# Kernel tuning notes

Measured on AMD Instinct MI355X. Metric: run time of the kernel, lower is better.

## Reference

```python
import jax, jax.numpy as jnp
import numpy as np

B, N, D, H = 32, 64, 256, 256
WORD_NUM, REL_NUM, POS_NUM, CAT_NUM = 50000, 50, 48, 5


def setup_inputs() -> dict:
    key = jax.random.key(0)
    ks = jax.random.split(key, 20)
    rng = np.random.default_rng(0)
    # valid dependency trees: head[i] < i, head[0] = -1 (root)
    heads_np = np.zeros((B, N), dtype=np.int32)
    for b in range(B):
        heads_np[b, 0] = -1
        for i in range(1, N):
            heads_np[b, i] = rng.integers(0, i)
    p = lambda k, shape: (0.02 * jax.random.normal(k, shape)).astype(jnp.float32)
    z = lambda shape: jnp.zeros(shape, jnp.float32)
    return {
        "xs": jax.random.randint(ks[0], (B, N), 0, WORD_NUM),
        "heads": jnp.asarray(heads_np),
        "rels": jax.random.randint(ks[1], (B, N), 0, REL_NUM),
        "labels": jax.random.randint(ks[2], (B, N), 0, WORD_NUM),
        "poss": jax.random.randint(ks[3], (B, N), 0, POS_NUM),
        "xlengths": jnp.full((B,), N, dtype=jnp.int32),
        "target_start": jnp.zeros((B,), jnp.int32),
        "target_end": jnp.full((B,), N - 1, jnp.int32),
        "x_mask": jnp.ones((B, N), jnp.float32),
        # parameters
        "emb_W": p(ks[4], (WORD_NUM, D)),
        "rel_W": p(ks[5], (REL_NUM, D)),
        "gru_Wi_f": p(ks[6], (2 * D, 3 * H)), "gru_Wh_f": p(ks[7], (H, 3 * H)),
        "gru_bi_f": z((3 * H,)), "gru_bh_f": z((3 * H,)),
        "gru_Wi_b": p(ks[8], (2 * D, 3 * H)), "gru_Wh_b": p(ks[9], (H, 3 * H)),
        "gru_bi_b": z((3 * H,)), "gru_bh_b": z((3 * H,)),
        "Wt": p(ks[10], (2 * H, D)), "bt": z((D,)),
        "dt_Wx": p(ks[11], (2 * D, 3 * H)), "dt_Uh": p(ks[12], (H, 3 * H)), "dt_b": z((3 * H,)),
        "td_Wx": p(ks[13], (2 * D, 3 * H)), "td_Uh": p(ks[14], (H, 3 * H)), "td_b": z((3 * H,)),
        "fc_W": p(ks[15], (2 * H, 100)), "fc_b": z((100,)),
        "fc2_W": p(ks[16], (100, CAT_NUM)), "fc2_b": z((CAT_NUM,)),
    }


def _gru_cell(xpt, hprev, Uh, bh):
    gh = hprev @ Uh + bh
    xr, xz, xn = jnp.split(xpt, 3, axis=-1)
    hr, hz, hn = jnp.split(gh, 3, axis=-1)
    r = jax.nn.sigmoid(xr + hr)
    zg = jax.nn.sigmoid(xz + hz)
    n = jnp.tanh(xn + r * hn)
    return (1.0 - zg) * n + zg * hprev


def _gru_dir(x, Wi, Wh, bi, bh):
    # x: [B,N,2D] -> hidden sequence [B,N,H]
    xp = x @ Wi + bi  # precompute input projections
    def step(h, xpt):
        hnew = _gru_cell(xpt, h, Wh, bh)
        return hnew, hnew
    h0 = jnp.zeros((x.shape[0], Wh.shape[0]), x.dtype)
    _, hs = jax.lax.scan(step, h0, jnp.swapaxes(xp, 0, 1))
    return jnp.swapaxes(hs, 0, 1)


def _dt_tree(inputs, heads, Wx, Uh, b):
    # bottom-up (child-sum) tree GRU; heads[b,i] < i so reversed order is topological
    Bn, Nn, _ = inputs.shape
    Hh = Uh.shape[0]
    xp = inputs @ Wx + b
    bar = jnp.arange(Bn)
    def step(carry, idx):
        C, Hout = carry  # C: accumulated child hidden sums [B,N,H]
        h = _gru_cell(xp[:, idx], C[:, idx], Uh, jnp.zeros((3 * Hh,), inputs.dtype))
        Hout = Hout.at[:, idx].set(h)
        par = heads[:, idx]
        valid = par >= 0
        C = C.at[bar, jnp.where(valid, par, 0)].add(jnp.where(valid[:, None], h, 0.0))
        return (C, Hout), None
    H0 = jnp.zeros((Bn, Nn, Hh), inputs.dtype)
    (_, Hout), _ = jax.lax.scan(step, (H0, H0), jnp.arange(Nn - 1, -1, -1))
    return Hout


def _td_tree(inputs, heads, Wx, Uh, b):
    # top-down tree GRU: parent hidden flows to children; index order 0..N-1 is topological
    Bn, Nn, _ = inputs.shape
    Hh = Uh.shape[0]
    xp = inputs @ Wx + b
    bar = jnp.arange(Bn)
    def step(Hout, idx):
        par = heads[:, idx]
        valid = par >= 0
        hp = jnp.where(valid[:, None], Hout[bar, jnp.where(valid, par, 0)], 0.0)
        h = _gru_cell(xp[:, idx], hp, Uh, jnp.zeros((3 * Hh,), inputs.dtype))
        Hout = Hout.at[:, idx].set(h)
        return Hout, None
    H0 = jnp.zeros((Bn, Nn, Hh), inputs.dtype)
    Hout, _ = jax.lax.scan(step, H0, jnp.arange(Nn))
    return Hout


def reference(xs, heads, rels, labels, poss, xlengths, target_start, target_end, x_mask,
              emb_W, rel_W,
              gru_Wi_f, gru_Wh_f, gru_bi_f, gru_bh_f,
              gru_Wi_b, gru_Wh_b, gru_bi_b, gru_bh_b,
              Wt, bt, dt_Wx, dt_Uh, dt_b, td_Wx, td_Uh, td_b,
              fc_W, fc_b, fc2_W, fc2_b):
    word_emb = emb_W[xs]
    label_emb = emb_W[labels]  # original uses self.embedding for labels too
    emb = jnp.concatenate([word_emb, label_emb], axis=-1)  # [B,N,2D]
    fwd = _gru_dir(emb, gru_Wi_f, gru_Wh_f, gru_bi_f, gru_bh_f)
    bwd = jnp.flip(_gru_dir(jnp.flip(emb, 1), gru_Wi_b, gru_Wh_b, gru_bi_b, gru_bh_b), 1)
    grus = jnp.concatenate([fwd, bwd], axis=-1) @ Wt + bt  # transform -> [B,N,D]
    rel_emb = rel_W[rels]
    outputs = jnp.concatenate([grus, rel_emb], axis=-1)  # [B,N,2D]
    dt_out = _dt_tree(outputs, heads, dt_Wx, dt_Uh, dt_b)
    td_out = _td_tree(outputs, heads, td_Wx, td_Uh, td_b)
    ctx = jnp.concatenate([dt_out, td_out], axis=-1)  # [B,N,2H]
    ctx = jnp.max(ctx, axis=1)  # max_pool1d over length -> [B,2H]
    ctx = ctx @ fc_W + fc_b
    ctx = ctx @ fc2_W + fc2_b
    return ctx
```

## Files before the change

### kernel.cpp

```cpp
#include <hip/hip_runtime.h>


typedef _Float16 half2v __attribute__((ext_vector_type(2)));
typedef _Float16 half8 __attribute__((ext_vector_type(8)));
typedef unsigned int u32x32 __attribute__((ext_vector_type(32)));
typedef float f32x4v __attribute__((ext_vector_type(4)));

__device__ __forceinline__ float fdot2f(unsigned a, unsigned b, float c) {
#if __has_builtin(__builtin_amdgcn_fdot2)
  return __builtin_amdgcn_fdot2(__builtin_bit_cast(half2v, a),
                                __builtin_bit_cast(half2v, b), c, false);
#else
  half2v av = __builtin_bit_cast(half2v, a), bv = __builtin_bit_cast(half2v, b);
  return c + (float)av.x * (float)bv.x + (float)av.y * (float)bv.y;
#endif
}

__device__ __forceinline__ unsigned packh2(float x, float y) {
  half2v p;
  p.x = (_Float16)x;
  p.y = (_Float16)y;
  return __builtin_bit_cast(unsigned, p);
}
__device__ __forceinline__ unsigned short f2u(float x) {
  return __builtin_bit_cast(unsigned short, (_Float16)x);
}
__device__ __forceinline__ float sigm(float x) { return 1.f / (1.f + __expf(-x)); }
__device__ __forceinline__ float tanh_fast(float x) {
  float cx = fminf(fmaxf(x, -15.f), 15.f);
  float e = __expf(2.f * cx);
  return (e - 1.f) / (e + 1.f);
}

__global__ __launch_bounds__(256) void pack_w(const float* __restrict__ W0,
                                              const float* __restrict__ W1,
                                              const float* __restrict__ W2,
                                              const float* __restrict__ W3, unsigned* P0,
                                              unsigned* P1, unsigned* P2, unsigned* P3) {
  const float* W;
  unsigned* P;
  switch (blockIdx.y) {
    case 0: W = W0; P = P0; break;
    case 1: W = W1; P = P1; break;
    case 2: W = W2; P = P2; break;
    default: W = W3; P = P3; break;
  }
  const int tid = blockIdx.x * 256 + threadIdx.x;
  const int i = tid & 3;
  const int u4 = tid >> 2;
  const int jg = u4 & 127;
  const int d4q = u4 >> 7;
  const int d4 = d4q % 48;
  const int q2 = d4q / 48;
  const int col2 = d4 / 24;
  const int rr = d4 % 24;
  const int g = rr >> 3;
  const int p4 = rr & 7;
  const int kp = p4 * 4 + i;
  const int k = q2 * 64 + kp * 2;
  const int col = g * 256 + col2 * 128 + jg;
  P[tid] = packh2(W[(size_t)k * 768 + col], W[(size_t)(k + 1) * 768 + col]);
}

__global__ __launch_bounds__(256) void tsplit(const float* __restrict__ W,
                                              unsigned short* __restrict__ WThi,
                                              unsigned short* __restrict__ WTlo, int K,
                                              int N) {
  __shared__ float T[32][33];
  const int ky = blockIdx.y * 32, nx = blockIdx.x * 32;
  const int r = threadIdx.x >> 3, c4 = (threadIdx.x & 7) * 4;
  float4 v = *(const float4*)(W + (size_t)(ky + r) * N + nx + c4);
  T[r][c4 + 0] = v.x;
  T[r][c4 + 1] = v.y;
  T[r][c4 + 2] = v.z;
  T[r][c4 + 3] = v.w;
  __syncthreads();
  float f[4] = {T[c4 + 0][r], T[c4 + 1][r], T[c4 + 2][r], T[c4 + 3][r]};
  ushort4 oh, ol;
  {
    _Float16 h0 = (_Float16)f[0], h1 = (_Float16)f[1], h2 = (_Float16)f[2],
             h3 = (_Float16)f[3];
    oh.x = __builtin_bit_cast(unsigned short, h0);
    oh.y = __builtin_bit_cast(unsigned short, h1);
    oh.z = __builtin_bit_cast(unsigned short, h2);
    oh.w = __builtin_bit_cast(unsigned short, h3);
    ol.x = f2u(f[0] - (float)h0);
    ol.y = f2u(f[1] - (float)h1);
    ol.z = f2u(f[2] - (float)h2);
    ol.w = f2u(f[3] - (float)h3);
  }
  *(ushort4*)(WThi + (size_t)(nx + r) * K + ky + c4) = oh;
  *(ushort4*)(WTlo + (size_t)(nx + r) * K + ky + c4) = ol;
}

__global__ void gather_emb_hl(const int* __restrict__ xs, const int* __restrict__ labels,
                              const float* __restrict__ embW,
                              unsigned short* __restrict__ eHi,
                              unsigned short* __restrict__ eLo) {
  const int row = blockIdx.x, t = threadIdx.x;
  const float4* W4 = (const float4*)embW;
  const int src = (t < 64) ? xs[row] : labels[row];
  float4 v = W4[(size_t)src * 64 + (t & 63)];
  float f[4] = {v.x, v.y, v.z, v.w};
  ushort4 oh, ol;
  _Float16 h0 = (_Float16)f[0], h1 = (_Float16)f[1], h2 = (_Float16)f[2],
           h3 = (_Float16)f[3];
  oh.x = __builtin_bit_cast(unsigned short, h0);
  oh.y = __builtin_bit_cast(unsigned short, h1);
  oh.z = __builtin_bit_cast(unsigned short, h2);
  oh.w = __builtin_bit_cast(unsigned short, h3);
  ol.x = f2u(f[0] - (float)h0);
  ol.y = f2u(f[1] - (float)h1);
  ol.z = f2u(f[2] - (float)h2);
  ol.w = f2u(f[3] - (float)h3);
  const size_t idx = (size_t)row * 512 + (t >> 6) * 256 + (t & 63) * 4;
  *(ushort4*)(eHi + idx) = oh;
  *(ushort4*)(eLo + idx) = ol;
}

__global__ void gather_rel_hl(const int* __restrict__ rels,
                              const float* __restrict__ relW,
                              unsigned short* __restrict__ oHi,
                              unsigned short* __restrict__ oLo) {
  const int row = blockIdx.x, t = threadIdx.x;
  const float4* W4 = (const float4*)relW;
  float4 v = W4[(size_t)rels[row] * 64 + t];
  float f[4] = {v.x, v.y, v.z, v.w};
  ushort4 oh, ol;
  _Float16 h0 = (_Float16)f[0], h1 = (_Float16)f[1], h2 = (_Float16)f[2],
           h3 = (_Float16)f[3];
  oh.x = __builtin_bit_cast(unsigned short, h0);
  oh.y = __builtin_bit_cast(unsigned short, h1);
  oh.z = __builtin_bit_cast(unsigned short, h2);
  oh.w = __builtin_bit_cast(unsigned short, h3);
  ol.x = f2u(f[0] - (float)h0);
  ol.y = f2u(f[1] - (float)h1);
  ol.z = f2u(f[2] - (float)h2);
  ol.w = f2u(f[3] - (float)h3);
  const size_t idx = (size_t)row * 512 + 256 + t * 4;
  *(ushort4*)(oHi + idx) = oh;
  *(ushort4*)(oLo + idx) = ol;
}

__global__ __launch_bounds__(256) void mm16p(
    const unsigned short* __restrict__ Ahi, const unsigned short* __restrict__ Alo,
    const unsigned short* __restrict__ Bhi, const unsigned short* __restrict__ Blo,
    const float* __restrict__ bias, float* __restrict__ Cf,
    unsigned short* __restrict__ CHi, unsigned short* __restrict__ CLo, int ldc,
    int mode) {
  __shared__ __align__(16) _Float16 As_h[64][40], As_l[64][40];
  __shared__ __align__(16) _Float16 Bs_h[64][40], Bs_l[64][40];
  const int t = threadIdx.x, l = t & 63, w = t >> 6;
  const int bm = blockIdx.y * 64, bn = blockIdx.x * 64;
  const int sr = t >> 2, sc = (t & 3) * 8;
  f32x4v ac0 = {0.f, 0.f, 0.f, 0.f}, ac1 = ac0, ac2 = ac0, ac3 = ac0;
  const int fr = w * 16 + (l & 15), fc = (l >> 4) * 8, lo16 = l & 15;
  for (int kt = 0; kt < 512; kt += 32) {
    *(uint4*)(&As_h[sr][sc]) = *(const uint4*)(Ahi + (size_t)(bm + sr) * 512 + kt + sc);
    *(uint4*)(&As_l[sr][sc]) = *(const uint4*)(Alo + (size_t)(bm + sr) * 512 + kt + sc);
    *(uint4*)(&Bs_h[sr][sc]) = *(const uint4*)(Bhi + (size_t)(bn + sr) * 512 + kt + sc);
    *(uint4*)(&Bs_l[sr][sc]) = *(const uint4*)(Blo + (size_t)(bn + sr) * 512 + kt + sc);
    __syncthreads();
    half8 avh = __builtin_bit_cast(half8, *(const uint4*)(&As_h[fr][fc]));
    half8 avl = __builtin_bit_cast(half8, *(const uint4*)(&As_l[fr][fc]));
#define BH(NT) __builtin_bit_cast(half8, *(const uint4*)(&Bs_h[(NT)*16 + lo16][fc]))
#define BL(NT) __builtin_bit_cast(half8, *(const uint4*)(&Bs_l[(NT)*16 + lo16][fc]))
    half8 b0h = BH(0), b1h = BH(1), b2h = BH(2), b3h = BH(3);
    half8 b0l = BL(0), b1l = BL(1), b2l = BL(2), b3l = BL(3);
#undef BH
#undef BL
    ac0 = __builtin_amdgcn_mfma_f32_16x16x32_f16(avh, b0h, ac0, 0, 0, 0);
    ac1 = __builtin_amdgcn_mfma_f32_16x16x32_f16(avh, b1h, ac1, 0, 0, 0);
    ac2 = __builtin_amdgcn_mfma_f32_16x16x32_f16(avh, b2h, ac2, 0, 0, 0);
    ac3 = __builtin_amdgcn_mfma_f32_16x16x32_f16(avh, b3h, ac3, 0, 0, 0);
    ac0 = __builtin_amdgcn_mfma_f32_16x16x32_f16(avh, b0l, ac0, 0, 0, 0);
    ac1 = __builtin_amdgcn_mfma_f32_16x16x32_f16(avh, b1l, ac1, 0, 0, 0);
    ac2 = __builtin_amdgcn_mfma_f32_16x16x32_f16(avh, b2l, ac2, 0, 0, 0);
    ac3 = __builtin_amdgcn_mfma_f32_16x16x32_f16(avh, b3l, ac3, 0, 0, 0);
    ac0 = __builtin_amdgcn_mfma_f32_16x16x32_f16(avl, b0h, ac0, 0, 0, 0);
    ac1 = __builtin_amdgcn_mfma_f32_16x16x32_f16(avl, b1h, ac1, 0, 0, 0);
    ac2 = __builtin_amdgcn_mfma_f32_16x16x32_f16(avl, b2h, ac2, 0, 0, 0);
    ac3 = __builtin_amdgcn_mfma_f32_16x16x32_f16(avl, b3h, ac3, 0, 0, 0);
    __syncthreads();
  }
  const int hi4 = l >> 4;
#define EPI(AC, NT)                                                            \
  {                                                                            \
    _Pragma("unroll") for (int i = 0; i < 4; ++i) {                            \
      const int row = bm + w * 16 + hi4 * 4 + i;                               \
      const int col = bn + (NT)*16 + lo16;                                     \
      float v = (AC)[i] + bias[col];                                           \
      if (mode == 0) {                                                         \
        Cf[(size_t)row * ldc + col] = v;                                       \
      } else {                                                                 \
        _Float16 h = (_Float16)v;                                              \
        CHi[(size_t)row * ldc + col] = __builtin_bit_cast(unsigned short, h);  \
        CLo[(size_t)row * ldc + col] = f2u(v - (float)h);                      \
      }                                                                        \
    }                                                                          \
  }
  EPI(ac0, 0) EPI(ac1, 1) EPI(ac2, 2) EPI(ac3, 3)
#undef EPI
}

__global__ __launch_bounds__(256) void mm16s_wt(const float* __restrict__ A,
                                                const float* __restrict__ W,
                                                const float* __restrict__ bias,
                                                unsigned short* __restrict__ CHi,
                                                unsigned short* __restrict__ CLo, int N,
                                                int ldc) {
  __shared__ __align__(16) _Float16 Ahi[64][40], Alo[64][40];
  __shared__ __align__(16) _Float16 Bhi[64][40], Blo[64][40];
  const int t = threadIdx.x, l = t & 63, w = t >> 6;
  const int bm = blockIdx.y * 64, bn = blockIdx.x * 64;
  const int ar = t >> 2, ac8 = (t & 3) * 8;
  const int bk = t >> 3, bn8 = (t & 7) * 8;
  f32x4v ac0 = {0.f, 0.f, 0.f, 0.f}, ac1 = ac0, ac2 = ac0, ac3 = ac0;
  const int fr = w * 16 + (l & 15), fc = (l >> 4) * 8, lo16 = l & 15;
  for (int kt = 0; kt < 512; kt += 32) {
    {
      const float* ap = A + (size_t)(bm + ar) * 512 + kt + ac8;
      float4 v0 = *(const float4*)ap;
      float4 v1 = *(const float4*)(ap + 4);
      float av[8] = {v0.x, v0.y, v0.z, v0.w, v1.x, v1.y, v1.z, v1.w};
#pragma unroll
      for (int i = 0; i < 8; ++i) {
        _Float16 h = (_Float16)av[i];
        Ahi[ar][ac8 + i] = h;
        Alo[ar][ac8 + i] = (_Float16)(av[i] - (float)h);
      }
    }
    {
      const float* wp = W + (size_t)(kt + bk) * N + bn + bn8;
      float4 v0 = *(const float4*)wp;
      float4 v1 = *(const float4*)(wp + 4);
      float wv[8] = {v0.x, v0.y, v0.z, v0.w, v1.x, v1.y, v1.z, v1.w};
#pragma unroll
      for (int i = 0; i < 8; ++i) {
        _Float16 h = (_Float16)wv[i];
        Bhi[bn8 + i][bk] = h;
        Blo[bn8 + i][bk] = (_Float16)(wv[i] - (float)h);
      }
    }
    __syncthreads();
    half8 avh = __builtin_bit_cast(half8, *(const uint4*)(&Ahi[fr][fc]));
    half8 avl = __builtin_bit_cast(half8, *(const uint4*)(&Alo[fr][fc]));
#define BH(NT) __builtin_bit_cast(half8, *(const uint4*)(&Bhi[(NT)*16 + lo16][fc]))
#define BL(NT) __builtin_bit_cast(half8, *(const uint4*)(&Blo[(NT)*16 + lo16][fc]))
    half8 b0h = BH(0), b1h = BH(1), b2h = BH(2), b3h = BH(3);
    half8 b0l = BL(0), b1l = BL(1), b2l = BL(2), b3l = BL(3);
#undef BH
#undef BL
    ac0 = __builtin_amdgcn_mfma_f32_16x16x32_f16(avh, b0h, ac0, 0, 0, 0);
    ac1 = __builtin_amdgcn_mfma_f32_16x16x32_f16(avh, b1h, ac1, 0, 0, 0);
    ac2 = __builtin_amdgcn_mfma_f32_16x16x32_f16(avh, b2h, ac2, 0, 0, 0);
    ac3 = __builtin_amdgcn_mfma_f32_16x16x32_f16(avh, b3h, ac3, 0, 0, 0);
    ac0 = __builtin_amdgcn_mfma_f32_16x16x32_f16(avh, b0l, ac0, 0, 0, 0);
    ac1 = __builtin_amdgcn_mfma_f32_16x16x32_f16(avh, b1l, ac1, 0, 0, 0);
    ac2 = __builtin_amdgcn_mfma_f32_16x16x32_f16(avh, b2l, ac2, 0, 0, 0);
    ac3 = __builtin_amdgcn_mfma_f32_16x16x32_f16(avh, b3l, ac3, 0, 0, 0);
    ac0 = __builtin_amdgcn_mfma_f32_16x16x32_f16(avl, b0h, ac0, 0, 0, 0);
    ac1 = __builtin_amdgcn_mfma_f32_16x16x32_f16(avl, b1h, ac1, 0, 0, 0);
    ac2 = __builtin_amdgcn_mfma_f32_16x16x32_f16(avl, b2h, ac2, 0, 0, 0);
    ac3 = __builtin_amdgcn_mfma_f32_16x16x32_f16(avl, b3h, ac3, 0, 0, 0);
    __syncthreads();
  }
  const int hi4 = l >> 4;
#define EPI(AC, NT)                                                            \
  {                                                                            \
    _Pragma("unroll") for (int i = 0; i < 4; ++i) {                            \
      const int row = bm + w * 16 + hi4 * 4 + i;                               \
      const int col = bn + (NT)*16 + lo16;                                     \
      float v = (AC)[i] + bias[col];                                           \
      _Float16 h = (_Float16)v;                                                \
      CHi[(size_t)row * ldc + col] = __builtin_bit_cast(unsigned short, h);    \
      CLo[(size_t)row * ldc + col] = f2u(v - (float)h);                        \
    }                                                                          \
  }
  EPI(ac0, 0) EPI(ac1, 1) EPI(ac2, 2) EPI(ac3, 3)
#undef EPI
}

template <int NP>
__device__ __forceinline__ void stage_w(const uint4* __restrict__ P4, int q2, int jg,
                                        int t, uint2 (*Wl)[512], u32x32& w0, u32x32& w1,
                                        u32x32& w2) {
#pragma unroll
  for (int p4 = 0; p4 < 8; ++p4) {
    uint4 v0 = P4[(q2 * 48 + p4) * 128 + jg];
    w0[4 * p4 + 0] = v0.x; w0[4 * p4 + 1] = v0.y;
    w0[4 * p4 + 2] = v0.z; w0[4 * p4 + 3] = v0.w;
    uint4 v1 = P4[(q2 * 48 + 8 + p4) * 128 + jg];
    w1[4 * p4 + 0] = v1.x; w1[4 * p4 + 1] = v1.y;
    w1[4 * p4 + 2] = v1.z; w1[4 * p4 + 3] = v1.w;
    uint4 v2 = P4[(q2 * 48 + 16 + p4) * 128 + jg];
    w2[4 * p4 + 0] = v2.x; w2[4 * p4 + 1] = v2.y;
    w2[4 * p4 + 2] = v2.z; w2[4 * p4 + 3] = v2.w;
  }
#pragma unroll
  for (int g = 0; g < 3; ++g)
#pragma unroll
    for (int p4 = 0; p4 < NP; ++p4) {
      uint4 v = P4[(q2 * 48 + 24 + g * 8 + p4) * 128 + jg];
      Wl[(g * NP + p4) * 2 + 0][t] = make_uint2(v.x, v.y);
      Wl[(g * NP + p4) * 2 + 1][t] = make_uint2(v.z, v.w);
    }
}

template <int NP>
__device__ __forceinline__ void dot_step(const u32x32& w0, const u32x32& w1,
                                         const u32x32& w2, const uint2 (*Wl)[512], int t,
                                         const uint4* __restrict__ P4, int sb,
                                         const uint4* hv4, float& a0, float& a1,
                                         float& a2, float& a3, float& a4, float& a5) {
#pragma unroll
  for (int c = 0; c < 8; ++c) {
    uint4 hu = hv4[c];
    a0 = fdot2f(w0[4 * c + 0], hu.x, a0); a0 = fdot2f(w0[4 * c + 1], hu.y, a0);
    a0 = fdot2f(w0[4 * c + 2], hu.z, a0); a0 = fdot2f(w0[4 * c + 3], hu.w, a0);
    a1 = fdot2f(w1[4 * c + 0], hu.x, a1); a1 = fdot2f(w1[4 * c + 1], hu.y, a1);
    a1 = fdot2f(w1[4 * c + 2], hu.z, a1); a1 = fdot2f(w1[4 * c + 3], hu.w, a1);
    a2 = fdot2f(w2[4 * c + 0], hu.x, a2); a2 = fdot2f(w2[4 * c + 1], hu.y, a2);
    a2 = fdot2f(w2[4 * c + 2], hu.z, a2); a2 = fdot2f(w2[4 * c + 3], hu.w, a2);
    if (c < NP) {
      uint2 u0 = Wl[(0 * NP + c) * 2 + 0][t], u1 = Wl[(0 * NP + c) * 2 + 1][t];
      a3 = fdot2f(u0.x, hu.x, a3); a3 = fdot2f(u0.y, hu.y, a3);
      a3 = fdot2f(u1.x, hu.z, a3); a3 = fdot2f(u1.y, hu.w, a3);
      uint2 v0 = Wl[(1 * NP + c) * 2 + 0][t], v1 = Wl[(1 * NP + c) * 2 + 1][t];
      a4 = fdot2f(v0.x, hu.x, a4); a4 = fdot2f(v0.y, hu.y, a4);
      a4 = fdot2f(v1.x, hu.z, a4); a4 = fdot2f(v1.y, hu.w, a4);
      uint2 x0 = Wl[(2 * NP + c) * 2 + 0][t], x1 = Wl[(2 * NP + c) * 2 + 1][t];
      a5 = fdot2f(x0.x, hu.x, a5); a5 = fdot2f(x0.y, hu.y, a5);
      a5 = fdot2f(x1.x, hu.z, a5); a5 = fdot2f(x1.y, hu.w, a5);
    } else {
      uint4 s0 = P4[sb + (0 * 8 + c) * 128];
      a3 = fdot2f(s0.x, hu.x, a3); a3 = fdot2f(s0.y, hu.y, a3);
      a3 = fdot2f(s0.z, hu.z, a3); a3 = fdot2f(s0.w, hu.w, a3);
      uint4 s1 = P4[sb + (1 * 8 + c) * 128];
      a4 = fdot2f(s1.x, hu.x, a4); a4 = fdot2f(s1.y, hu.y, a4);
      a4 = fdot2f(s1.z, hu.z, a4); a4 = fdot2f(s1.w, hu.w, a4);
      uint4 s2 = P4[sb + (2 * 8 + c) * 128];
      a5 = fdot2f(s2.x, hu.x, a5); a5 = fdot2f(s2.y, hu.y, a5);
      a5 = fdot2f(s2.z, hu.z, a5); a5 = fdot2f(s2.w, hu.w, a5);
    }
  }
}

__global__ __launch_bounds__(512) void gru_scan_h(
    const unsigned* __restrict__ Pf, const unsigned* __restrict__ Pb,
    const float* __restrict__ bh_f, const float* __restrict__ bh_b,
    const float* __restrict__ xp_f, const float* __restrict__ xp_b,
    float* __restrict__ grus) {
  const int b = blockIdx.x & 31, dir = blockIdx.x >> 5;
  const uint4* __restrict__ P4 = (const uint4*)(dir ? Pb : Pf);
  const float* __restrict__ bh = dir ? bh_b : bh_f;
  const float* __restrict__ xp = dir ? xp_b : xp_f;

  __shared__ uint2 Wl[36][512];
  __shared__ float part[4][3][256];
  __shared__ __align__(16) unsigned h2[128];

  const int t = threadIdx.x, jg = t & 127, q2 = t >> 7;
  const int sb = (q2 * 48 + 24) * 128 + jg;

  u32x32 w0, w1, w2;
  stage_w<6>(P4, q2, jg, t, Wl, w0, w1, w2);

  float br0 = 0.f, br1 = 0.f, bz0 = 0.f, bz1 = 0.f, bn0 = 0.f, bn1 = 0.f;
  float hp0 = 0.f, hp1 = 0.f;
  if (t < 128) {
    br0 = bh[2 * t];       br1 = bh[2 * t + 1];
    bz0 = bh[256 + 2 * t]; bz1 = bh[256 + 2 * t + 1];
    bn0 = bh[512 + 2 * t]; bn1 = bh[512 + 2 * t + 1];
    h2[t] = 0u;
  }
  __syncthreads();

  for (int s = 0; s < 64; ++s) {
    const int nn = dir ? (63 - s) : s;
    float2 pxr, pxz, pxn;
    if (t < 128) {
      const float* xrow = xp + (size_t)(b * 64 + nn) * 768;
      pxr = *(const float2*)(xrow + 2 * t);
      pxz = *(const float2*)(xrow + 256 + 2 * t);
      pxn = *(const float2*)(xrow + 512 + 2 * t);
    }
    float a0 = 0.f, a1 = 0.f, a2 = 0.f, a3 = 0.f, a4 = 0.f, a5 = 0.f;
    dot_step<6>(w0, w1, w2, Wl, t, P4, sb, (const uint4*)(h2 + q2 * 32), a0, a1, a2, a3,
                a4, a5);
    part[q2][0][jg] = a0;
    part[q2][0][128 + jg] = a3;
    part[q2][1][jg] = a1;
    part[q2][1][128 + jg] = a4;
    part[q2][2][jg] = a2;
    part[q2][2][128 + jg] = a5;
    __syncthreads();
    if (t < 128) {
      float s0r = 0, s1r = 0, s0z = 0, s1z = 0, s0n = 0, s1n = 0;
#pragma unroll
      for (int q = 0; q < 4; ++q) {
        float2 pr = *(const float2*)(&part[q][0][2 * t]); s0r += pr.x; s1r += pr.y;
        float2 pz = *(const float2*)(&part[q][1][2 * t]); s0z += pz.x; s1z += pz.y;
        float2 pn = *(const float2*)(&part[q][2][2 * t]); s0n += pn.x; s1n += pn.y;
      }
      float r0 = sigm(pxr.x + s0r + br0), r1 = sigm(pxr.y + s1r + br1);
      float z0 = sigm(pxz.x + s0z + bz0), z1 = sigm(pxz.y + s1z + bz1);
      float n0 = tanh_fast(pxn.x + r0 * (s0n + bn0));
      float n1 = tanh_fast(pxn.y + r1 * (s1n + bn1));
      float h0 = (1.f - z0) * n0 + z0 * hp0;
      float h1 = (1.f - z1) * n1 + z1 * hp1;
      hp0 = h0;
      hp1 = h1;
      h2[t] = packh2(h0, h1);
      float2 o;
      o.x = h0;
      o.y = h1;
      *(float2*)(grus + (size_t)(b * 64 + nn) * 512 + dir * 256 + 2 * t) = o;
    }
    __syncthreads();
  }
}

__global__ __launch_bounds__(512) void tree_scan_h(
    const unsigned* __restrict__ Pdt, const unsigned* __restrict__ Ptd,
    const float* __restrict__ xp_dt, const float* __restrict__ xp_td,
    const int* __restrict__ heads, float* __restrict__ ctx) {
  const int b = blockIdx.x & 31, istd = blockIdx.x >> 5;
  const uint4* __restrict__ P4 = (const uint4*)(istd ? Ptd : Pdt);
  const float* __restrict__ xp = istd ? xp_td : xp_dt;

  __shared__ float S[65][256];
  __shared__ __align__(16) unsigned S2[65][128];
  __shared__ uint2 Wl[12][512];
  __shared__ float part[4][3][256];
  __shared__ int hd[64];

  const int t = threadIdx.x, jg = t & 127, q2 = t >> 7;
  const int sb = (q2 * 48 + 24) * 128 + jg;

  u32x32 w0, w1, w2;
  stage_w<2>(P4, q2, jg, t, Wl, w0, w1, w2);

  for (int i = t; i < 65 * 256; i += 512) (&S[0][0])[i] = 0.f;
  for (int i = t; i < 65 * 128; i += 512) (&S2[0][0])[i] = 0u;
  if (t < 64) hd[t] = heads[b * 64 + t];
  __syncthreads();

  float mx0 = -1e30f, mx1 = -1e30f;

  for (int s = 0; s < 64; ++s) {
    const int idx = istd ? s : (63 - s);
    const int par = hd[idx];
    const int srow = istd ? (par >= 0 ? par : 64) : idx;

    float2 pxr, pxz, pxn;
    if (t < 128) {
      const float* xrow = xp + (size_t)(b * 64 + idx) * 768;
      pxr = *(const float2*)(xrow + 2 * t);
      pxz = *(const float2*)(xrow + 256 + 2 * t);
      pxn = *(const float2*)(xrow + 512 + 2 * t);
    }
    float a0 = 0.f, a1 = 0.f, a2 = 0.f, a3 = 0.f, a4 = 0.f, a5 = 0.f;
    dot_step<2>(w0, w1, w2, Wl, t, P4, sb, (const uint4*)(&S2[srow][q2 * 32]), a0, a1,
                a2, a3, a4, a5);
    part[q2][0][jg] = a0;
    part[q2][0][128 + jg] = a3;
    part[q2][1][jg] = a1;
    part[q2][1][128 + jg] = a4;
    part[q2][2][jg] = a2;
    part[q2][2][128 + jg] = a5;
    __syncthreads();
    if (t < 128) {
      float s0r = 0, s1r = 0, s0z = 0, s1z = 0, s0n = 0, s1n = 0;
#pragma unroll
      for (int q = 0; q < 4; ++q) {
        float2 pr = *(const float2*)(&part[q][0][2 * t]); s0r += pr.x; s1r += pr.y;
        float2 pz = *(const float2*)(&part[q][1][2 * t]); s0z += pz.x; s1z += pz.y;
        float2 pn = *(const float2*)(&part[q][2][2 * t]); s0n += pn.x; s1n += pn.y;
      }
      float r0 = sigm(pxr.x + s0r), r1 = sigm(pxr.y + s1r);
      float z0 = sigm(pxz.x + s0z), z1 = sigm(pxz.y + s1z);
      float n0 = tanh_fast(pxn.x + r0 * s0n), n1 = tanh_fast(pxn.y + r1 * s1n);
      float hp0 = S[srow][2 * t], hp1 = S[srow][2 * t + 1];
      float h0 = (1.f - z0) * n0 + z0 * hp0;
      float h1 = (1.f - z1) * n1 + z1 * hp1;
      mx0 = fmaxf(mx0, h0);
      mx1 = fmaxf(mx1, h1);
      if (istd) {
        S[idx][2 * t] = h0;
        S[idx][2 * t + 1] = h1;
        S2[idx][t] = packh2(h0, h1);
      } else if (par >= 0) {
        float c0 = S[par][2 * t] + h0;
        float c1 = S[par][2 * t + 1] + h1;
        S[par][2 * t] = c0;
        S[par][2 * t + 1] = c1;
        S2[par][t] = packh2(c0, c1);
      }
    }
    __syncthreads();
  }

  if (t < 128) {
    float2 o;
    o.x = mx0;
    o.y = mx1;
    *(float2*)(ctx + (size_t)b * 512 + istd * 256 + 2 * t) = o;
  }
}

__global__ __launch_bounds__(128) void final_k(const float* __restrict__ ctx_g,
                                               const float* __restrict__ fcW,
                                               const float* __restrict__ fcb,
                                               const float* __restrict__ fc2W,
                                               const float* __restrict__ fc2b,
                                               float* __restrict__ out) {
  const int b = blockIdx.x, t = threadIdx.x;
  __shared__ float ctx[512];
  __shared__ float f1[100];
  for (int i = t; i < 512; i += 128) ctx[i] = ctx_g[(size_t)b * 512 + i];
  __syncthreads();
  if (t < 100) {
    float a = fcb[t];
    for (int k = 0; k < 512; ++k) a = fmaf(ctx[k], fcW[k * 100 + t], a);
    f1[t] = a;
  }
  __syncthreads();
  if (t < 5) {
    float a = fc2b[t];
    for (int k = 0; k < 100; ++k) a = fmaf(f1[k], fc2W[k * 5 + t], a);
    out[b * 5 + t] = a;
  }
}

extern "C" void kernel_launch(void* const* d_in, const int* in_sizes, int n_in, void* d_out,
                              int out_size, void* d_ws, size_t ws_size, hipStream_t stream) {
  const int* xs = (const int*)d_in[0];
  const int* heads = (const int*)d_in[1];
  const int* rels = (const int*)d_in[2];
  const int* labels = (const int*)d_in[3];
  const float* emb_W = (const float*)d_in[9];
  const float* rel_W = (const float*)d_in[10];
  const float* Wi_f = (const float*)d_in[11];
  const float* Wh_f = (const float*)d_in[12];
  const float* bi_f = (const float*)d_in[13];
  const float* bh_f = (const float*)d_in[14];
  const float* Wi_b = (const float*)d_in[15];
  const float* Wh_b = (const float*)d_in[16];
  const float* bi_b = (const float*)d_in[17];
  const float* bh_b = (const float*)d_in[18];
  const float* Wt = (const float*)d_in[19];
  const float* bt = (const float*)d_in[20];
  const float* dt_Wx = (const float*)d_in[21];
  const float* dt_Uh = (const float*)d_in[22];
  const float* dt_b = (const float*)d_in[23];
  const float* td_Wx = (const float*)d_in[24];
  const float* td_Uh = (const float*)d_in[25];
  const float* td_b = (const float*)d_in[26];
  const float* fc_W = (const float*)d_in[27];
  const float* fc_b = (const float*)d_in[28];
  const float* fc2_W = (const float*)d_in[29];
  const float* fc2_b = (const float*)d_in[30];

  float* ws = (float*)d_ws;
  float* xp_f = ws;
  float* xp_b = ws + 1572864;
  float* grus = ws + 3145728;
  float* ctx = ws + 4194304;
  unsigned* P0 = (unsigned*)(ws + 4210688);
  unsigned* P1 = P0 + 98304;
  unsigned* P2 = P1 + 98304;
  unsigned* P3 = P2 + 98304;
  unsigned short* embHi = (unsigned short*)(ws + 4603904);
  unsigned short* embLo = (unsigned short*)(ws + 5128192);
  unsigned short* WTh_a = (unsigned short*)(ws + 5652480);
  unsigned short* WTl_a = (unsigned short*)(ws + 5849088);
  unsigned short* WTh_b = (unsigned short*)(ws + 6045696);
  unsigned short* WTl_b = (unsigned short*)(ws + 6242304);
  unsigned short* outHi = embHi;
  unsigned short* outLo = embLo;

  pack_w<<<dim3(384, 4), 256, 0, stream>>>(Wh_f, Wh_b, dt_Uh, td_Uh, P0, P1, P2, P3);
  tsplit<<<dim3(24, 16), 256, 0, stream>>>(Wi_f, WTh_a, WTl_a, 512, 768);
  tsplit<<<dim3(24, 16), 256, 0, stream>>>(Wi_b, WTh_b, WTl_b, 512, 768);
  gather_emb_hl<<<2048, 128, 0, stream>>>(xs, labels, emb_W, embHi, embLo);
  mm16p<<<dim3(12, 32), 256, 0, stream>>>(embHi, embLo, WTh_a, WTl_a, bi_f, xp_f,
                                          nullptr, nullptr, 768, 0);
  mm16p<<<dim3(12, 32), 256, 0, stream>>>(embHi, embLo, WTh_b, WTl_b, bi_b, xp_b,
                                          nullptr, nullptr, 768, 0);
  gru_scan_h<<<64, 512, 0, stream>>>(P0, P1, bh_f, bh_b, xp_f, xp_b, grus);
  tsplit<<<dim3(24, 16), 256, 0, stream>>>(dt_Wx, WTh_a, WTl_a, 512, 768);
  tsplit<<<dim3(24, 16), 256, 0, stream>>>(td_Wx, WTh_b, WTl_b, 512, 768);
  mm16s_wt<<<dim3(4, 32), 256, 0, stream>>>(grus, Wt, bt, outHi, outLo, 256, 512);
  gather_rel_hl<<<2048, 64, 0, stream>>>(rels, rel_W, outHi, outLo);
  mm16p<<<dim3(12, 32), 256, 0, stream>>>(outHi, outLo, WTh_a, WTl_a, dt_b, xp_f,
                                          nullptr, nullptr, 768, 0);
  mm16p<<<dim3(12, 32), 256, 0, stream>>>(outHi, outLo, WTh_b, WTl_b, td_b, xp_b,
                                          nullptr, nullptr, 768, 0);
  tree_scan_h<<<64, 512, 0, stream>>>(P2, P3, xp_f, xp_b, heads, ctx);
  final_k<<<32, 128, 0, stream>>>(ctx, fc_W, fc_b, fc2_W, fc2_b, (float*)d_out);
}
```

Baseline: 328.0 us.

## Move tree-scan fp32 state to global memory to stage more weights in LDS

The tree scan kernel's fp32 hidden-state array S moves from shared memory to a per-block global workspace. The freed LDS holds twice as many recurrent weight slices (stage_w/dot_step<4>), which cuts per-step global weight reads. The prior-state loads are issued before the dot product so their latency overlaps the matvec. Separately, the paired tsplit launches are merged into one launch using blockIdx.z. The risk is that global-memory round trips for state on the serial dependency chain add latency, and the Sg workspace reuses the embHi region that is no longer needed.

Result: no change. 325.8 us (-0.7%).

```diff
diff --git a/kernel.cpp b/kernel.cpp
--- a/kernel.cpp
+++ b/kernel.cpp
@@ -62,10 +62,16 @@
   P[tid] = packh2(W[(size_t)k * 768 + col], W[(size_t)(k + 1) * 768 + col]);
 }
 
-__global__ __launch_bounds__(256) void tsplit(const float* __restrict__ W,
-                                              unsigned short* __restrict__ WThi,
-                                              unsigned short* __restrict__ WTlo, int K,
-                                              int N) {
+__global__ __launch_bounds__(256) void tsplit2(const float* __restrict__ W0,
+                                               const float* __restrict__ W1,
+                                               unsigned short* __restrict__ H0,
+                                               unsigned short* __restrict__ L0,
+                                               unsigned short* __restrict__ H1,
+                                               unsigned short* __restrict__ L1, int K,
+                                               int N) {
+  const float* __restrict__ W = blockIdx.z ? W1 : W0;
+  unsigned short* __restrict__ WThi = blockIdx.z ? H1 : H0;
+  unsigned short* __restrict__ WTlo = blockIdx.z ? L1 : L0;
   __shared__ float T[32][33];
   const int ky = blockIdx.y * 32, nx = blockIdx.x * 32;
   const int r = threadIdx.x >> 3, c4 = (threadIdx.x & 7) * 4;
@@ -421,17 +427,17 @@
   }
 }
 
-__global__ __launch_bounds__(512) void tree_scan_h(
+__global__ __launch_bounds__(512) void tree_scan_g(
     const unsigned* __restrict__ Pdt, const unsigned* __restrict__ Ptd,
     const float* __restrict__ xp_dt, const float* __restrict__ xp_td,
-    const int* __restrict__ heads, float* __restrict__ ctx) {
+    const int* __restrict__ heads, float* __restrict__ ctx, float* __restrict__ Sg) {
   const int b = blockIdx.x & 31, istd = blockIdx.x >> 5;
   const uint4* __restrict__ P4 = (const uint4*)(istd ? Ptd : Pdt);
   const float* __restrict__ xp = istd ? xp_td : xp_dt;
-
-  __shared__ float S[65][256];
+  float* __restrict__ S = Sg + (size_t)blockIdx.x * 16384;
+
   __shared__ __align__(16) unsigned S2[65][128];
-  __shared__ uint2 Wl[12][512];
+  __shared__ uint2 Wl[24][512];
   __shared__ float part[4][3][256];
   __shared__ int hd[64];
 
@@ -439,9 +445,9 @@
   const int sb = (q2 * 48 + 24) * 128 + jg;
 
   u32x32 w0, w1, w2;
-  stage_w<2>(P4, q2, jg, t, Wl, w0, w1, w2);
-
-  for (int i = t; i < 65 * 256; i += 512) (&S[0][0])[i] = 0.f;
+  stage_w<4>(P4, q2, jg, t, Wl, w0, w1, w2);
+
+  for (int i = t; i < 16384; i += 512) S[i] = 0.f;
   for (int i = t; i < 65 * 128; i += 512) (&S2[0][0])[i] = 0u;
   if (t < 64) hd[t] = heads[b * 64 + t];
   __syncthreads();
@@ -454,14 +460,31 @@
     const int srow = istd ? (par >= 0 ? par : 64) : idx;
 
     float2 pxr, pxz, pxn;
+    float hp0 = 0.f, hp1 = 0.f, acc0 = 0.f, acc1 = 0.f;
     if (t < 128) {
       const float* xrow = xp + (size_t)(b * 64 + idx) * 768;
       pxr = *(const float2*)(xrow + 2 * t);
       pxz = *(const float2*)(xrow + 256 + 2 * t);
       pxn = *(const float2*)(xrow + 512 + 2 * t);
+      if (istd) {
+        if (par >= 0) {
+          float2 v = *(const float2*)(S + par * 256 + 2 * t);
+          hp0 = v.x;
+          hp1 = v.y;
+        }
+      } else {
+        float2 v = *(const float2*)(S + idx * 256 + 2 * t);
+        hp0 = v.x;
+        hp1 = v.y;
+        if (par >= 0) {
+          float2 a = *(const float2*)(S + par * 256 + 2 * t);
+          acc0 = a.x;
+          acc1 = a.y;
+        }
+      }
     }
     float a0 = 0.f, a1 = 0.f, a2 = 0.f, a3 = 0.f, a4 = 0.f, a5 = 0.f;
-    dot_step<2>(w0, w1, w2, Wl, t, P4, sb, (const uint4*)(&S2[srow][q2 * 32]), a0, a1,
+    dot_step<4>(w0, w1, w2, Wl, t, P4, sb, (const uint4*)(&S2[srow][q2 * 32]), a0, a1,
                 a2, a3, a4, a5);
     part[q2][0][jg] = a0;
     part[q2][0][128 + jg] = a3;
@@ -481,20 +504,23 @@
       float r0 = sigm(pxr.x + s0r), r1 = sigm(pxr.y + s1r);
       float z0 = sigm(pxz.x + s0z), z1 = sigm(pxz.y + s1z);
       float n0 = tanh_fast(pxn.x + r0 * s0n), n1 = tanh_fast(pxn.y + r1 * s1n);
-      float hp0 = S[srow][2 * t], hp1 = S[srow][2 * t + 1];
       float h0 = (1.f - z0) * n0 + z0 * hp0;
       float h1 = (1.f - z1) * n1 + z1 * hp1;
       mx0 = fmaxf(mx0, h0);
       mx1 = fmaxf(mx1, h1);
       if (istd) {
-        S[idx][2 * t] = h0;
-        S[idx][2 * t + 1] = h1;
+        float2 o;
+        o.x = h0;
+        o.y = h1;
+        *(float2*)(S + idx * 256 + 2 * t) = o;
         S2[idx][t] = packh2(h0, h1);
       } else if (par >= 0) {
-        float c0 = S[par][2 * t] + h0;
-        float c1 = S[par][2 * t + 1] + h1;
-        S[par][2 * t] = c0;
-        S[par][2 * t + 1] = c1;
+        float c0 = acc0 + h0;
+        float c1 = acc1 + h1;
+        float2 o;
+        o.x = c0;
+        o.y = c1;
+        *(float2*)(S + par * 256 + 2 * t) = o;
         S2[par][t] = packh2(c0, c1);
       }
     }
@@ -579,24 +605,25 @@
   unsigned short* WTl_b = (unsigned short*)(ws + 6242304);
   unsigned short* outHi = embHi;
   unsigned short* outLo = embLo;
+  float* Sg = ws + 4603904;
 
   pack_w<<<dim3(384, 4), 256, 0, stream>>>(Wh_f, Wh_b, dt_Uh, td_Uh, P0, P1, P2, P3);
-  tsplit<<<dim3(24, 16), 256, 0, stream>>>(Wi_f, WTh_a, WTl_a, 512, 768);
-  tsplit<<<dim3(24, 16), 256, 0, stream>>>(Wi_b, WTh_b, WTl_b, 512, 768);
+  tsplit2<<<dim3(24, 16, 2), 256, 0, stream>>>(Wi_f, Wi_b, WTh_a, WTl_a, WTh_b, WTl_b,
+                                               512, 768);
   gather_emb_hl<<<2048, 128, 0, stream>>>(xs, labels, emb_W, embHi, embLo);
   mm16p<<<dim3(12, 32), 256, 0, stream>>>(embHi, embLo, WTh_a, WTl_a, bi_f, xp_f,
                                           nullptr, nullptr, 768, 0);
   mm16p<<<dim3(12, 32), 256, 0, stream>>>(embHi, embLo, WTh_b, WTl_b, bi_b, xp_b,
                                           nullptr, nullptr, 768, 0);
   gru_scan_h<<<64, 512, 0, stream>>>(P0, P1, bh_f, bh_b, xp_f, xp_b, grus);
-  tsplit<<<dim3(24, 16), 256, 0, stream>>>(dt_Wx, WTh_a, WTl_a, 512, 768);
-  tsplit<<<dim3(24, 16), 256, 0, stream>>>(td_Wx, WTh_b, WTl_b, 512, 768);
+  tsplit2<<<dim3(24, 16, 2), 256, 0, stream>>>(dt_Wx, td_Wx, WTh_a, WTl_a, WTh_b, WTl_b,
+                                               512, 768);
   mm16s_wt<<<dim3(4, 32), 256, 0, stream>>>(grus, Wt, bt, outHi, outLo, 256, 512);
   gather_rel_hl<<<2048, 64, 0, stream>>>(rels, rel_W, outHi, outLo);
   mm16p<<<dim3(12, 32), 256, 0, stream>>>(outHi, outLo, WTh_a, WTl_a, dt_b, xp_f,
                                           nullptr, nullptr, 768, 0);
   mm16p<<<dim3(12, 32), 256, 0, stream>>>(outHi, outLo, WTh_b, WTl_b, td_b, xp_b,
                                           nullptr, nullptr, 768, 0);
-  tree_scan_h<<<64, 512, 0, stream>>>(P2, P3, xp_f, xp_b, heads, ctx);
+  tree_scan_g<<<64, 512, 0, stream>>>(P2, P3, xp_f, xp_b, heads, ctx, Sg);
   final_k<<<32, 128, 0, stream>>>(ctx, fc_W, fc_b, fc2_W, fc2_b, (float*)d_out);
 }
```
